# Kernel optimization log

Hardware: AMD Instinct MI355X
Metric: run time of the kernel (lower is better)

## Reference

```python
import jax, jax.numpy as jnp
import numpy as np

B, H, W, R, C = 4, 64, 64, 64, 32  # batch, height, width, in-channels r, conv out-channels


def setup_inputs() -> dict:
    key = jax.random.key(0)
    kx, kf, kg = jax.random.split(key, 3)
    x = jax.random.normal(kx, (B, H, W, R), dtype=jnp.float32)
    # 1x1 conv with in_channels=1: kernel is effectively a length-C vector
    w_f = jax.random.normal(kf, (C,), dtype=jnp.float32) * 0.1
    w_g = jax.random.normal(kg, (C,), dtype=jnp.float32) * 0.1
    gamma = jnp.ones((), dtype=jnp.float32)
    return {"x": x, "w_f": w_f, "w_g": w_g, "gamma": gamma}


def reference(x, w_f, w_g, gamma):
    b, h, w, r = x.shape
    hw = h * w
    xs = x.reshape(b, hw, r)                      # [B, HW, R]
    # conv_f / conv_g: each scalar of xs times weight vector -> [B, HW, R*C]
    x_f = (xs[..., None] * w_f).reshape(b, hw, -1)
    x_g = (xs[..., None] * w_g).reshape(b, hw, -1)
    attn = jnp.einsum('bik,bjk->bij', x_f, x_g)   # [B, HW, HW]
    attn = jax.nn.softmax(attn, axis=-1) * gamma
    # out[b,j,r] = sum_i attn[b,j,i] * xs[b,i,r]
    out = jnp.einsum('bji,bir->bjr', attn, xs)
    return out.reshape(b, h, w, r)
```

## Files before the change

### kernel.cpp

```cpp
#include <hip/hip_runtime.h>


#define N_SEQ 4096
#define KS    8
#define LOG2E 1.4426950408889634f

typedef __attribute__((ext_vector_type(8))) short short8;
typedef __attribute__((ext_vector_type(4))) short short4v;
typedef __attribute__((ext_vector_type(4))) float f4;
typedef __attribute__((ext_vector_type(16))) float f32x16;
typedef _Float16 half8  __attribute__((ext_vector_type(8)));
typedef _Float16 half2t __attribute__((ext_vector_type(2)));
typedef __fp16   fp16x2 __attribute__((ext_vector_type(2)));

union U8  { short8 v8; short4v v4[2]; unsigned short u[8]; };
union PKU { fp16x2 f; half2t h; unsigned int u; };
union US  { short8 s; half8 h; };
union W4U { unsigned int u[4]; half8 h; };

#define MFMA16(a,b,c)  __builtin_amdgcn_mfma_f32_16x16x32_bf16(a,b,c,0,0,0)
#define MFMA32F(a,b,c) __builtin_amdgcn_mfma_f32_32x32x16_f16(a,b,c,0,0,0)

static __device__ __forceinline__ unsigned short f2bf(float f){
  unsigned int u = __float_as_uint(f);
  u += 0x7fffu + ((u>>16)&1u);
  return (unsigned short)(u>>16);
}
static __device__ __forceinline__ float bf2f(unsigned short b){
  return __uint_as_float(((unsigned int)b)<<16);
}
static __device__ __forceinline__ unsigned int pk_u32(float a, float b){
#if __has_builtin(__builtin_amdgcn_cvt_pkrtz)
  PKU u; u.f = __builtin_amdgcn_cvt_pkrtz(a, b); return u.u;
#else
  PKU u; u.h.x = (_Float16)a; u.h.y = (_Float16)b; return u.u;
#endif
}
static __device__ __forceinline__ float fexp2(float x){
#if __has_builtin(__builtin_amdgcn_exp2f)
  return __builtin_amdgcn_exp2f(x);
#else
  return exp2f(x);
#endif
}
static __device__ __forceinline__ f4 splat4(float v){ f4 r; r.x=v; r.y=v; r.z=v; r.w=v; return r; }
static __device__ __forceinline__ f4 exp2v(f4 v){
  f4 r; r.x=fexp2(v.x); r.y=fexp2(v.y); r.z=fexp2(v.z); r.w=fexp2(v.w); return r;
}
static __device__ __forceinline__ f4 max4(f4 a, f4 b){
  f4 r; r.x=fmaxf(a.x,b.x); r.y=fmaxf(a.y,b.y); r.z=fmaxf(a.z,b.z); r.w=fmaxf(a.w,b.w); return r;
}
static __device__ __forceinline__ f4 shx4(f4 v, int m){
  f4 r; r.x=__shfl_xor(v.x,m,64); r.y=__shfl_xor(v.y,m,64);
        r.z=__shfl_xor(v.z,m,64); r.w=__shfl_xor(v.w,m,64); return r;
}
static __device__ __forceinline__ f32x16 zero16(){
  f32x16 z;
  #pragma unroll
  for (int i = 0; i < 16; ++i) z[i] = 0.f;
  return z;
}
static __device__ __forceinline__ void gload16(const unsigned short* g, unsigned short* l){
  __builtin_amdgcn_global_load_lds((const __attribute__((address_space(1))) void*)g,
                                   (__attribute__((address_space(3))) void*)l, 16, 0, 0);
}
static __device__ __forceinline__ half8 mkfrag(unsigned int Da0, unsigned int Da1,
                                               unsigned int Db0, unsigned int Db1, bool hib){
  const unsigned int e0 = __shfl_xor(hib ? Da0 : Db0, 32, 64);
  const unsigned int e1 = __shfl_xor(hib ? Da1 : Db1, 32, 64);
  W4U w;
  w.u[0] = hib ? e0  : Da0;
  w.u[1] = hib ? e1  : Da1;
  w.u[2] = hib ? Db0 : e0;
  w.u[3] = hib ? Db1 : e1;
  return w.h;
}

__global__ __launch_bounds__(256) void prep6_kernel(
    const float* __restrict__ x,
    unsigned short* __restrict__ XF, unsigned short* __restrict__ VF)
{
  __shared__ __align__(16) unsigned short T [64][82];
  __shared__ __align__(16) unsigned short TT[64][82];
  const int tid  = threadIdx.x;
  const int bb   = blockIdx.x >> 6;
  const int tile = blockIdx.x & 63;
  {
    const int r  = tid >> 2;
    const int c4 = tid & 3;
    const float* src = x + ((size_t)(bb*N_SEQ + tile*64 + r))*64 + c4*16;
    unsigned short h[16];
    #pragma unroll
    for (int i = 0; i < 4; ++i) {
      const float4 f = *(const float4*)(src + i*4);
      const unsigned int u0 = pk_u32(f.x, f.y);
      const unsigned int u1 = pk_u32(f.z, f.w);
      h[i*4+0] = (unsigned short)(u0 & 0xffffu);
      h[i*4+1] = (unsigned short)(u0 >> 16);
      h[i*4+2] = (unsigned short)(u1 & 0xffffu);
      h[i*4+3] = (unsigned short)(u1 >> 16);
    }
    #pragma unroll
    for (int j = 0; j < 16; ++j) T[r][c4*16+j] = h[j];
    #pragma unroll
    for (int j = 0; j < 16; ++j) TT[c4*16+j][r] = h[j];
  }
  __syncthreads();
  const size_t ob = ((size_t)(bb*64 + tile)) * 4096;
  #pragma unroll
  for (int s0 = 0; s0 < 2; ++s0) {
    const int s  = s0*256 + tid;
    const int fb = s >> 6;
    const int l  = s & 63;
    const int rr = (fb >> 2)*32 + (l & 31);
    const int cc = (fb & 3)*16 + (l >> 5)*8;
    U8 a, b;
    #pragma unroll
    for (int j = 0; j < 8; ++j) { a.u[j] = T[rr][cc+j]; b.u[j] = TT[rr][cc+j]; }
    *(short8*)(XF + ob + (size_t)s*8) = a.v8;
    *(short8*)(VF + ob + (size_t)s*8) = b.v8;
  }
}

__global__ __launch_bounds__(256, 2) void fattn8_kernel(
    const float* __restrict__ wf, const float* __restrict__ wg,
    const unsigned short* __restrict__ XF, const unsigned short* __restrict__ VF,
    float* __restrict__ OP, float* __restrict__ LP)
{
  __shared__ __align__(16) unsigned short KL[2][4096];
  __shared__ __align__(16) unsigned short VL[2][4096];

  const int tid  = threadIdx.x;
  const int lane = tid & 63;
  const int wv   = tid >> 6;
  const int l31  = lane & 31;
  const int hi   = lane >> 5;
  const bool hib = hi != 0;
  const int ks   = blockIdx.x >> 6;
  const int rem  = blockIdx.x & 63;
  const int bb   = rem >> 4;
  const int qP   = rem & 15;

  float s = 0.f;
  #pragma unroll
  for (int i = 0; i < 32; ++i) s += wf[i]*wg[i];
  const float s2 = s * LOG2E;
  const _Float16 s2h = (_Float16)s2;

  half8 qf[2][4];
  {
    const unsigned short* xq = XF + ((size_t)(bb*64 + qP*4 + wv))*4096 + lane*8;
    half8 sv;
    #pragma unroll
    for (int j = 0; j < 8; ++j) sv[j] = s2h;
    #pragma unroll
    for (int qg = 0; qg < 2; ++qg)
      #pragma unroll
      for (int kst = 0; kst < 4; ++kst) {
        US u; u.s = *(const short8*)(xq + (qg*4+kst)*512);
        qf[qg][kst] = u.h * sv;
      }
  }

  f32x16 Oc[2][2];
  #pragma unroll
  for (int qg = 0; qg < 2; ++qg)
    #pragma unroll
    for (int dg = 0; dg < 2; ++dg) Oc[qg][dg] = zero16();
  float lacc[2] = {0.f, 0.f};

  const unsigned short* gK = XF + ((size_t)(bb*64 + ks*8))*4096;
  const unsigned short* gV = VF + ((size_t)(bb*64 + ks*8))*4096;

  #pragma unroll
  for (int c = 0; c < 2; ++c) {
    gload16(gK + (c*256+tid)*8, &KL[0][(c*256+tid)*8]);
    gload16(gV + (c*256+tid)*8, &VL[0][(c*256+tid)*8]);
  }
  __syncthreads();

  #pragma unroll 1
  for (int it = 0; it < 8; ++it) {
    const int cur = it & 1;
    if (it + 1 < 8) {
      #pragma unroll
      for (int c = 0; c < 2; ++c) {
        gload16(gK + (it+1)*4096 + (c*256+tid)*8, &KL[cur^1][(c*256+tid)*8]);
        gload16(gV + (it+1)*4096 + (c*256+tid)*8, &VL[cur^1][(c*256+tid)*8]);
      }
    }
    const unsigned short* KB = &KL[cur][0];
    const unsigned short* VB = &VL[cur][0];

    #pragma unroll
    for (int kg = 0; kg < 2; ++kg) {
      half8 kf[4];
      #pragma unroll
      for (int kst = 0; kst < 4; ++kst) {
        US u; u.s = *(const short8*)(KB + ((kg*4+kst)*64 + lane)*8);
        kf[kst] = u.h;
      }
      f32x16 St[2];
      St[0] = zero16(); St[1] = zero16();
      __builtin_amdgcn_s_setprio(1);
      #pragma unroll
      for (int kst = 0; kst < 4; ++kst) {
        St[0] = MFMA32F(kf[kst], qf[0][kst], St[0]);
        St[1] = MFMA32F(kf[kst], qf[1][kst], St[1]);
      }
      __builtin_amdgcn_s_setprio(0);

      half8 pa[2][2];
      #pragma unroll
      for (int qg = 0; qg < 2; ++qg) {
        float p[16];
        float sm = 0.f;
        #pragma unroll
        for (int r = 0; r < 16; ++r) { p[r] = fexp2(St[qg][r]); sm += p[r]; }
        lacc[qg] += sm;
        const unsigned int D0 = pk_u32(p[0],  p[1]);
        const unsigned int D1 = pk_u32(p[2],  p[3]);
        const unsigned int D2 = pk_u32(p[4],  p[5]);
        const unsigned int D3 = pk_u32(p[6],  p[7]);
        const unsigned int D4 = pk_u32(p[8],  p[9]);
        const unsigned int D5 = pk_u32(p[10], p[11]);
        const unsigned int D6 = pk_u32(p[12], p[13]);
        const unsigned int D7 = pk_u32(p[14], p[15]);
        pa[qg][0] = mkfrag(D0, D1, D2, D3, hib);
        pa[qg][1] = mkfrag(D4, D5, D6, D7, hib);
      }

      __builtin_amdgcn_s_setprio(1);
      #pragma unroll
      for (int dg = 0; dg < 2; ++dg) {
        US v0, v1;
        v0.s = *(const short8*)(VB + ((dg*4 + kg*2 + 0)*64 + lane)*8);
        v1.s = *(const short8*)(VB + ((dg*4 + kg*2 + 1)*64 + lane)*8);
        #pragma unroll
        for (int qg = 0; qg < 2; ++qg) {
          Oc[qg][dg] = MFMA32F(pa[qg][0], v0.h, Oc[qg][dg]);
          Oc[qg][dg] = MFMA32F(pa[qg][1], v1.h, Oc[qg][dg]);
        }
      }
      __builtin_amdgcn_s_setprio(0);
    }
    __syncthreads();
  }

  lacc[0] += __shfl_xor(lacc[0], 32, 64);
  lacc[1] += __shfl_xor(lacc[1], 32, 64);

  float* op = OP + (size_t)blockIdx.x * (256*64);
  #pragma unroll
  for (int qg = 0; qg < 2; ++qg) {
    #pragma unroll
    for (int dg = 0; dg < 2; ++dg) {
      #pragma unroll
      for (int r = 0; r < 16; ++r) {
        const int row = wv*64 + qg*32 + (r & 3) + 8*(r >> 2) + 4*hi;
        op[row*64 + dg*32 + l31] = Oc[qg][dg][r];
      }
    }
    if (hi == 0)
      LP[(size_t)blockIdx.x*256 + wv*64 + qg*32 + l31] = lacc[qg];
  }
}

__global__ __launch_bounds__(256) void merge8_kernel(
    const float* __restrict__ OP, const float* __restrict__ LP,
    const float* __restrict__ gm, float* __restrict__ out)
{
  const int idx = blockIdx.x*256 + threadIdx.x;
  const int e0  = idx*4;
  const int d0  = e0 & 63;
  const int q   = e0 >> 6;
  const int bb  = q >> 12;
  const int qq  = q & 4095;
  const int qP  = qq >> 8;
  const int row = qq & 255;
  float4 acc = make_float4(0.f,0.f,0.f,0.f);
  float l = 0.f;
  #pragma unroll
  for (int sct = 0; sct < KS; ++sct) {
    const int blk = sct*64 + bb*16 + qP;
    const float4 o = *(const float4*)(OP + (size_t)blk*16384 + row*64 + d0);
    acc.x += o.x; acc.y += o.y; acc.z += o.z; acc.w += o.w;
    l += LP[(size_t)blk*256 + row];
  }
  const float w = gm[0] / l;
  float4 r; r.x = acc.x*w; r.y = acc.y*w; r.z = acc.z*w; r.w = acc.w*w;
  *(float4*)(out + e0) = r;
}

#define LDKF 72
#define TILEF (64*LDKF)
#define LDP 36

__global__ __launch_bounds__(256) void fattn_fallback(
    const float* __restrict__ x, const float* __restrict__ wf,
    const float* __restrict__ wg, const float* __restrict__ gm,
    float* __restrict__ out)
{
  __shared__ __align__(16) unsigned short KHI[2*TILEF];
  __shared__ __align__(16) unsigned short KLO[2*TILEF];
  __shared__ __align__(16) unsigned short VT [2*TILEF];
  __shared__ __align__(16) unsigned short PB [4*32*LDP];

  const int tid  = threadIdx.x;
  const int lane = tid & 63;
  const int wv   = tid >> 6;
  const int mg   = wv & 1;
  const int hh   = wv >> 1;
  const int quad = lane >> 4;
  const int l15  = lane & 15;
  const int bb   = blockIdx.x >> 6;
  const int qb   = (blockIdx.x & 63) << 6;

  float s = 0.f;
  #pragma unroll
  for (int i = 0; i < 32; ++i) s += wf[i]*wg[i];
  const float s2 = s * LOG2E;
  const float gamma = gm[0];

  const float* xb = x + ((size_t)bb * N_SEQ) * 64;

  short8 qhf[2][2], qlf[2][2];
  #pragma unroll
  for (int mt = 0; mt < 2; ++mt) {
    const int row = qb + mg*32 + mt*16 + l15;
    #pragma unroll
    for (int c = 0; c < 2; ++c) {
      const float* src = xb + row*64 + c*32 + quad*8;
      const float4 a0 = *(const float4*)src;
      const float4 a1 = *(const float4*)(src+4);
      float qv[8] = {a0.x,a0.y,a0.z,a0.w,a1.x,a1.y,a1.z,a1.w};
      U8 vh, vl;
      #pragma unroll
      for (int j = 0; j < 8; ++j) {
        float q = qv[j]*s2;
        unsigned short hb = f2bf(q);
        vh.u[j] = (short)hb;
        vl.u[j] = (short)f2bf(q - bf2f(hb));
      }
      qhf[mt][c] = vh.v8; qlf[mt][c] = vl.v8;
    }
  }

  f4 Oc[2][4], mo[2], ls[2];
  #pragma unroll
  for (int mt = 0; mt < 2; ++mt) {
    mo[mt] = splat4(-1e30f);
    ls[mt] = splat4(0.f);
    #pragma unroll
    for (int nt = 0; nt < 4; ++nt) Oc[mt][nt] = splat4(0.f);
  }

  const int sh   = tid >> 7;
  const int srow = (tid & 127) >> 1;
  const int sch  = tid & 1;

  float4 sr[8];
  {
    const float* sp = xb + (sh*2048 + srow)*64 + sch*32;
    #pragma unroll
    for (int i = 0; i < 8; ++i) sr[i] = *(const float4*)(sp + i*4);
    unsigned short hb[32], lb[32];
    #pragma unroll
    for (int i = 0; i < 8; ++i) {
      float vv[4] = {sr[i].x, sr[i].y, sr[i].z, sr[i].w};
      #pragma unroll
      for (int j = 0; j < 4; ++j) {
        unsigned short h = f2bf(vv[j]);
        hb[i*4+j] = h;
        lb[i*4+j] = f2bf(vv[j] - bf2f(h));
      }
    }
    const int kbase = sh*TILEF + srow*LDKF + sch*32;
    #pragma unroll
    for (int g = 0; g < 4; ++g) {
      U8 wh, wl;
      #pragma unroll
      for (int j = 0; j < 8; ++j) { wh.u[j]=(short)hb[g*8+j]; wl.u[j]=(short)lb[g*8+j]; }
      *(short8*)&KHI[kbase+g*8] = wh.v8;
      *(short8*)&KLO[kbase+g*8] = wl.v8;
    }
    #pragma unroll
    for (int j = 0; j < 32; ++j) VT[sh*TILEF + (sch*32+j)*LDKF + srow] = hb[j];
  }
  __syncthreads();

  #pragma unroll 1
  for (int t = 0; t < 32; ++t) {
    if (t+1 < 32) {
      const float* sp = xb + (sh*2048 + (t+1)*64 + srow)*64 + sch*32;
      #pragma unroll
      for (int i = 0; i < 8; ++i) sr[i] = *(const float4*)(sp + i*4);
    }

    f4 Sa[2][4];
    #pragma unroll
    for (int mt = 0; mt < 2; ++mt)
      #pragma unroll
      for (int n = 0; n < 4; ++n) Sa[mt][n] = splat4(0.f);

    const int kldsb = hh*TILEF;
    #pragma unroll
    for (int n = 0; n < 4; ++n) {
      #pragma unroll
      for (int c = 0; c < 2; ++c) {
        const int off = kldsb + (n*16 + l15)*LDKF + c*32 + quad*8;
        const short8 bh = *(const short8*)&KHI[off];
        const short8 bl = *(const short8*)&KLO[off];
        #pragma unroll
        for (int mt = 0; mt < 2; ++mt) {
          Sa[mt][n] = MFMA16(qhf[mt][c], bh, Sa[mt][n]);
          Sa[mt][n] = MFMA16(qlf[mt][c], bh, Sa[mt][n]);
          Sa[mt][n] = MFMA16(qhf[mt][c], bl, Sa[mt][n]);
        }
      }
    }

    f4 p[2][4];
    #pragma unroll
    for (int mt = 0; mt < 2; ++mt) {
      f4 rm = max4(max4(Sa[mt][0],Sa[mt][1]), max4(Sa[mt][2],Sa[mt][3]));
      rm = max4(rm, shx4(rm,1));
      rm = max4(rm, shx4(rm,2));
      rm = max4(rm, shx4(rm,4));
      rm = max4(rm, shx4(rm,8));
      f4 mn = max4(mo[mt], rm);
      f4 al = exp2v(mo[mt] - mn);
      mo[mt] = mn;
      f4 rs = splat4(0.f);
      #pragma unroll
      for (int n = 0; n < 4; ++n) { p[mt][n] = exp2v(Sa[mt][n] - mn); rs += p[mt][n]; }
      rs += shx4(rs,1); rs += shx4(rs,2); rs += shx4(rs,4); rs += shx4(rs,8);
      ls[mt] = ls[mt]*al + rs;
      #pragma unroll
      for (int nt = 0; nt < 4; ++nt) Oc[mt][nt] *= al;
    }

    const int pw = wv * (32*LDP);
    #pragma unroll
    for (int kc = 0; kc < 2; ++kc) {
      #pragma unroll
      for (int mt = 0; mt < 2; ++mt) {
        #pragma unroll
        for (int n2 = 0; n2 < 2; ++n2) {
          const f4 pv = p[mt][kc*2+n2];
          const int base = pw + (mt*16 + quad*4)*LDP + n2*16 + l15;
          ((unsigned short*)PB)[base        ] = f2bf(pv.x);
          ((unsigned short*)PB)[base +   LDP] = f2bf(pv.y);
          ((unsigned short*)PB)[base + 2*LDP] = f2bf(pv.z);
          ((unsigned short*)PB)[base + 3*LDP] = f2bf(pv.w);
        }
      }
      short8 pa[2];
      #pragma unroll
      for (int mt = 0; mt < 2; ++mt) {
        U8 u;
        const int rb = pw + (mt*16 + l15)*LDP + quad*8;
        u.v4[0] = *(const short4v*)&((unsigned short*)PB)[rb];
        u.v4[1] = *(const short4v*)&((unsigned short*)PB)[rb+4];
        pa[mt] = u.v8;
      }
      #pragma unroll
      for (int nt = 0; nt < 4; ++nt) {
        const short8 vb = *(const short8*)&VT[kldsb + (nt*16 + l15)*LDKF + kc*32 + quad*8];
        #pragma unroll
        for (int mt = 0; mt < 2; ++mt) Oc[mt][nt] = MFMA16(pa[mt], vb, Oc[mt][nt]);
      }
    }

    __syncthreads();

    if (t+1 < 32) {
      unsigned short hb[32], lb[32];
      #pragma unroll
      for (int i = 0; i < 8; ++i) {
        float vv[4] = {sr[i].x, sr[i].y, sr[i].z, sr[i].w};
        #pragma unroll
        for (int j = 0; j < 4; ++j) {
          unsigned short h = f2bf(vv[j]);
          hb[i*4+j] = h;
          lb[i*4+j] = f2bf(vv[j] - bf2f(h));
        }
      }
      const int kbase = sh*TILEF + srow*LDKF + sch*32;
      #pragma unroll
      for (int g = 0; g < 4; ++g) {
        U8 wh, wl;
        #pragma unroll
        for (int j = 0; j < 8; ++j) { wh.u[j]=(short)hb[g*8+j]; wl.u[j]=(short)lb[g*8+j]; }
        *(short8*)&KHI[kbase+g*8] = wh.v8;
        *(short8*)&KLO[kbase+g*8] = wl.v8;
      }
      #pragma unroll
      for (int j = 0; j < 32; ++j) VT[sh*TILEF + (sch*32+j)*LDKF + srow] = hb[j];
      __syncthreads();
    }
  }

  float* MO  = (float*)KHI;
  float* MML = (float*)KLO;
  if (hh == 1) {
    #pragma unroll
    for (int mt = 0; mt < 2; ++mt) {
      const int rbase = mg*32 + mt*16 + quad*4;
      #pragma unroll
      for (int nt = 0; nt < 4; ++nt) {
        MO[(rbase+0)*64 + nt*16 + l15] = Oc[mt][nt].x;
        MO[(rbase+1)*64 + nt*16 + l15] = Oc[mt][nt].y;
        MO[(rbase+2)*64 + nt*16 + l15] = Oc[mt][nt].z;
        MO[(rbase+3)*64 + nt*16 + l15] = Oc[mt][nt].w;
      }
      if (l15 == 0) {
        MML[rbase+0] = mo[mt].x; MML[rbase+1] = mo[mt].y;
        MML[rbase+2] = mo[mt].z; MML[rbase+3] = mo[mt].w;
        MML[64+rbase+0] = ls[mt].x; MML[64+rbase+1] = ls[mt].y;
        MML[64+rbase+2] = ls[mt].z; MML[64+rbase+3] = ls[mt].w;
      }
    }
  }
  __syncthreads();
  if (hh == 0) {
    #pragma unroll
    for (int mt = 0; mt < 2; ++mt) {
      const int rbase = mg*32 + mt*16 + quad*4;
      f4 m1, l1;
      m1.x = MML[rbase+0]; m1.y = MML[rbase+1]; m1.z = MML[rbase+2]; m1.w = MML[rbase+3];
      l1.x = MML[64+rbase+0]; l1.y = MML[64+rbase+1]; l1.z = MML[64+rbase+2]; l1.w = MML[64+rbase+3];
      const f4 mn = max4(mo[mt], m1);
      const f4 a0 = exp2v(mo[mt] - mn);
      const f4 a1 = exp2v(m1 - mn);
      f4 lt = ls[mt]*a0 + l1*a1;
      f4 w; w.x = gamma/lt.x; w.y = gamma/lt.y; w.z = gamma/lt.z; w.w = gamma/lt.w;
      #pragma unroll
      for (int nt = 0; nt < 4; ++nt) {
        #pragma unroll
        for (int rg = 0; rg < 4; ++rg) {
          const int rr = rbase + rg;
          const float o1 = MO[rr*64 + nt*16 + l15];
          const float val = (Oc[mt][nt][rg]*a0[rg] + o1*a1[rg]) * w[rg];
          out[((size_t)bb*N_SEQ + qb + rr)*64 + nt*16 + l15] = val;
        }
      }
    }
  }
}

extern "C" void kernel_launch(void* const* d_in, const int* in_sizes, int n_in,
                              void* d_out, int out_size, void* d_ws, size_t ws_size,
                              hipStream_t stream) {
  const float* x  = (const float*)d_in[0];
  const float* wf = (const float*)d_in[1];
  const float* wg = (const float*)d_in[2];
  const float* gm = (const float*)d_in[3];
  float* out = (float*)d_out;

  const size_t XF_OFF = 0;
  const size_t VF_OFF = 2097152;
  const size_t OP_OFF = 4194304;
  const size_t LP_OFF = OP_OFF + (size_t)512*256*64*4;
  const size_t NEED   = LP_OFF + (size_t)512*256*4;

  if (ws_size >= NEED) {
    unsigned short* XFp = (unsigned short*)((char*)d_ws + XF_OFF);
    unsigned short* VFp = (unsigned short*)((char*)d_ws + VF_OFF);
    float* OP = (float*)((char*)d_ws + OP_OFF);
    float* LP = (float*)((char*)d_ws + LP_OFF);
    prep6_kernel<<<dim3(256), dim3(256), 0, stream>>>(x, XFp, VFp);
    fattn8_kernel<<<dim3(512), dim3(256), 0, stream>>>(wf, wg, XFp, VFp, OP, LP);
    merge8_kernel<<<dim3(1024), dim3(256), 0, stream>>>(OP, LP, gm, out);
  } else {
    fattn_fallback<<<dim3(256), dim3(256), 0, stream>>>(x, wf, wg, gm, out);
  }
}
```

Before: 93.75 us.

## Replace global split-K with intra-block wave split and fused merge

The attention kernel no longer splits the key sequence across 8 blocks that write partial outputs and row sums to global memory for a separate merge kernel. Instead, 256 blocks of 512 threads each own 64 queries and sweep all keys. Waves are split by key parity, key group and query group, and their partial results are reduced through shared memory before the kernel writes normalized output directly. This removes the merge launch and the global round-trip of partials, in exchange for fewer, larger blocks, a 65 KB shared buffer, and longer serial loops per block.

```diff
diff --git a/kernel.cpp b/kernel.cpp
--- a/kernel.cpp
+++ b/kernel.cpp
@@ -2,7 +2,6 @@
 
 
 #define N_SEQ 4096
-#define KS    8
 #define LOG2E 1.4426950408889634f
 
 typedef __attribute__((ext_vector_type(8))) short short8;
@@ -122,13 +121,16 @@
   }
 }
 
-__global__ __launch_bounds__(256, 2) void fattn8_kernel(
+__global__ __launch_bounds__(512, 2) void fattn9_kernel(
     const float* __restrict__ wf, const float* __restrict__ wg,
+    const float* __restrict__ gm,
     const unsigned short* __restrict__ XF, const unsigned short* __restrict__ VF,
-    float* __restrict__ OP, float* __restrict__ LP)
+    float* __restrict__ out)
 {
-  __shared__ __align__(16) unsigned short KL[2][4096];
-  __shared__ __align__(16) unsigned short VL[2][4096];
+  __shared__ __align__(16) unsigned char SMEM[66560];
+  unsigned short* TLE  = (unsigned short*)SMEM;
+  float*          LO   = (float*)SMEM;
+  float*          LSUM = (float*)(SMEM + 65536);
 
   const int tid  = threadIdx.x;
   const int lane = tid & 63;
@@ -136,10 +138,11 @@
   const int l31  = lane & 31;
   const int hi   = lane >> 5;
   const bool hib = hi != 0;
-  const int ks   = blockIdx.x >> 6;
-  const int rem  = blockIdx.x & 63;
-  const int bb   = rem >> 4;
-  const int qP   = rem & 15;
+  const int par  = wv >> 2;
+  const int kg   = (wv >> 1) & 1;
+  const int qg   = wv & 1;
+  const int bb   = blockIdx.x >> 6;
+  const int qt   = blockIdx.x & 63;
 
   float s = 0.f;
   #pragma unroll
@@ -147,149 +150,125 @@
   const float s2 = s * LOG2E;
   const _Float16 s2h = (_Float16)s2;
 
-  half8 qf[2][4];
+  half8 qf[4];
   {
-    const unsigned short* xq = XF + ((size_t)(bb*64 + qP*4 + wv))*4096 + lane*8;
+    const unsigned short* xq = XF + ((size_t)(bb*64 + qt))*4096 + lane*8;
     half8 sv;
     #pragma unroll
     for (int j = 0; j < 8; ++j) sv[j] = s2h;
     #pragma unroll
-    for (int qg = 0; qg < 2; ++qg)
-      #pragma unroll
-      for (int kst = 0; kst < 4; ++kst) {
-        US u; u.s = *(const short8*)(xq + (qg*4+kst)*512);
-        qf[qg][kst] = u.h * sv;
-      }
-  }
-
-  f32x16 Oc[2][2];
-  #pragma unroll
-  for (int qg = 0; qg < 2; ++qg)
-    #pragma unroll
-    for (int dg = 0; dg < 2; ++dg) Oc[qg][dg] = zero16();
-  float lacc[2] = {0.f, 0.f};
-
-  const unsigned short* gK = XF + ((size_t)(bb*64 + ks*8))*4096;
-  const unsigned short* gV = VF + ((size_t)(bb*64 + ks*8))*4096;
-
-  #pragma unroll
-  for (int c = 0; c < 2; ++c) {
-    gload16(gK + (c*256+tid)*8, &KL[0][(c*256+tid)*8]);
-    gload16(gV + (c*256+tid)*8, &VL[0][(c*256+tid)*8]);
-  }
+    for (int kst = 0; kst < 4; ++kst) {
+      US u; u.s = *(const short8*)(xq + (qg*4+kst)*512);
+      qf[kst] = u.h * sv;
+    }
+  }
+
+  f32x16 Oc[2];
+  Oc[0] = zero16(); Oc[1] = zero16();
+  float lacc = 0.f;
+
+  const unsigned short* gK = XF + (size_t)bb*64*4096;
+  const unsigned short* gV = VF + (size_t)bb*64*4096;
+
+  #define STAGE(p, b)                                                            \
+    _Pragma("unroll")                                                            \
+    for (int c = 0; c < 4; ++c) {                                                \
+      const unsigned short* src =                                                \
+        ((c >> 1) ? gV : gK) + ((size_t)((p)*2 + (c & 1)))*4096 + tid*8;         \
+      unsigned short* dst = TLE + ((((b)*2 + (c & 1))*2 + (c >> 1))*4096) + tid*8;\
+      gload16(src, dst);                                                         \
+    }
+
+  STAGE(0, 0);
   __syncthreads();
 
   #pragma unroll 1
-  for (int it = 0; it < 8; ++it) {
+  for (int it = 0; it < 32; ++it) {
     const int cur = it & 1;
-    if (it + 1 < 8) {
-      #pragma unroll
-      for (int c = 0; c < 2; ++c) {
-        gload16(gK + (it+1)*4096 + (c*256+tid)*8, &KL[cur^1][(c*256+tid)*8]);
-        gload16(gV + (it+1)*4096 + (c*256+tid)*8, &VL[cur^1][(c*256+tid)*8]);
-      }
-    }
-    const unsigned short* KB = &KL[cur][0];
-    const unsigned short* VB = &VL[cur][0];
-
-    #pragma unroll
-    for (int kg = 0; kg < 2; ++kg) {
-      half8 kf[4];
-      #pragma unroll
-      for (int kst = 0; kst < 4; ++kst) {
-        US u; u.s = *(const short8*)(KB + ((kg*4+kst)*64 + lane)*8);
-        kf[kst] = u.h;
-      }
-      f32x16 St[2];
-      St[0] = zero16(); St[1] = zero16();
-      __builtin_amdgcn_s_setprio(1);
-      #pragma unroll
-      for (int kst = 0; kst < 4; ++kst) {
-        St[0] = MFMA32F(kf[kst], qf[0][kst], St[0]);
-        St[1] = MFMA32F(kf[kst], qf[1][kst], St[1]);
-      }
-      __builtin_amdgcn_s_setprio(0);
-
-      half8 pa[2][2];
-      #pragma unroll
-      for (int qg = 0; qg < 2; ++qg) {
-        float p[16];
-        float sm = 0.f;
-        #pragma unroll
-        for (int r = 0; r < 16; ++r) { p[r] = fexp2(St[qg][r]); sm += p[r]; }
-        lacc[qg] += sm;
-        const unsigned int D0 = pk_u32(p[0],  p[1]);
-        const unsigned int D1 = pk_u32(p[2],  p[3]);
-        const unsigned int D2 = pk_u32(p[4],  p[5]);
-        const unsigned int D3 = pk_u32(p[6],  p[7]);
-        const unsigned int D4 = pk_u32(p[8],  p[9]);
-        const unsigned int D5 = pk_u32(p[10], p[11]);
-        const unsigned int D6 = pk_u32(p[12], p[13]);
-        const unsigned int D7 = pk_u32(p[14], p[15]);
-        pa[qg][0] = mkfrag(D0, D1, D2, D3, hib);
-        pa[qg][1] = mkfrag(D4, D5, D6, D7, hib);
-      }
-
-      __builtin_amdgcn_s_setprio(1);
-      #pragma unroll
-      for (int dg = 0; dg < 2; ++dg) {
-        US v0, v1;
-        v0.s = *(const short8*)(VB + ((dg*4 + kg*2 + 0)*64 + lane)*8);
-        v1.s = *(const short8*)(VB + ((dg*4 + kg*2 + 1)*64 + lane)*8);
-        #pragma unroll
-        for (int qg = 0; qg < 2; ++qg) {
-          Oc[qg][dg] = MFMA32F(pa[qg][0], v0.h, Oc[qg][dg]);
-          Oc[qg][dg] = MFMA32F(pa[qg][1], v1.h, Oc[qg][dg]);
-        }
-      }
-      __builtin_amdgcn_s_setprio(0);
-    }
+    if (it + 1 < 32) { STAGE(it + 1, cur ^ 1); }
+
+    const unsigned short* KB = TLE + ((cur*2 + par)*2 + 0)*4096;
+    const unsigned short* VB = KB + 4096;
+
+    half8 kf[4];
+    #pragma unroll
+    for (int kst = 0; kst < 4; ++kst) {
+      US u; u.s = *(const short8*)(KB + ((kg*4+kst)*64 + lane)*8);
+      kf[kst] = u.h;
+    }
+    f32x16 St = zero16();
+    __builtin_amdgcn_s_setprio(1);
+    #pragma unroll
+    for (int kst = 0; kst < 4; ++kst) St = MFMA32F(kf[kst], qf[kst], St);
+    __builtin_amdgcn_s_setprio(0);
+
+    float p[16];
+    float sm = 0.f;
+    #pragma unroll
+    for (int r = 0; r < 16; ++r) { p[r] = fexp2(St[r]); sm += p[r]; }
+    lacc += sm;
+    const unsigned int D0 = pk_u32(p[0],  p[1]);
+    const unsigned int D1 = pk_u32(p[2],  p[3]);
+    const unsigned int D2 = pk_u32(p[4],  p[5]);
+    const unsigned int D3 = pk_u32(p[6],  p[7]);
+    const unsigned int D4 = pk_u32(p[8],  p[9]);
+    const unsigned int D5 = pk_u32(p[10], p[11]);
+    const unsigned int D6 = pk_u32(p[12], p[13]);
+    const unsigned int D7 = pk_u32(p[14], p[15]);
+    half8 pa0 = mkfrag(D0, D1, D2, D3, hib);
+    half8 pa1 = mkfrag(D4, D5, D6, D7, hib);
+
+    __builtin_amdgcn_s_setprio(1);
+    #pragma unroll
+    for (int dg = 0; dg < 2; ++dg) {
+      US v0, v1;
+      v0.s = *(const short8*)(VB + ((dg*4 + kg*2 + 0)*64 + lane)*8);
+      v1.s = *(const short8*)(VB + ((dg*4 + kg*2 + 1)*64 + lane)*8);
+      Oc[dg] = MFMA32F(pa0, v0.h, Oc[dg]);
+      Oc[dg] = MFMA32F(pa1, v1.h, Oc[dg]);
+    }
+    __builtin_amdgcn_s_setprio(0);
+
     __syncthreads();
   }
 
-  lacc[0] += __shfl_xor(lacc[0], 32, 64);
-  lacc[1] += __shfl_xor(lacc[1], 32, 64);
-
-  float* op = OP + (size_t)blockIdx.x * (256*64);
-  #pragma unroll
-  for (int qg = 0; qg < 2; ++qg) {
-    #pragma unroll
-    for (int dg = 0; dg < 2; ++dg) {
-      #pragma unroll
-      for (int r = 0; r < 16; ++r) {
-        const int row = wv*64 + qg*32 + (r & 3) + 8*(r >> 2) + 4*hi;
-        op[row*64 + dg*32 + l31] = Oc[qg][dg][r];
-      }
-    }
-    if (hi == 0)
-      LP[(size_t)blockIdx.x*256 + wv*64 + qg*32 + l31] = lacc[qg];
-  }
-}
-
-__global__ __launch_bounds__(256) void merge8_kernel(
-    const float* __restrict__ OP, const float* __restrict__ LP,
-    const float* __restrict__ gm, float* __restrict__ out)
-{
-  const int idx = blockIdx.x*256 + threadIdx.x;
-  const int e0  = idx*4;
-  const int d0  = e0 & 63;
-  const int q   = e0 >> 6;
-  const int bb  = q >> 12;
-  const int qq  = q & 4095;
-  const int qP  = qq >> 8;
-  const int row = qq & 255;
-  float4 acc = make_float4(0.f,0.f,0.f,0.f);
-  float l = 0.f;
-  #pragma unroll
-  for (int sct = 0; sct < KS; ++sct) {
-    const int blk = sct*64 + bb*16 + qP;
-    const float4 o = *(const float4*)(OP + (size_t)blk*16384 + row*64 + d0);
-    acc.x += o.x; acc.y += o.y; acc.z += o.z; acc.w += o.w;
-    l += LP[(size_t)blk*256 + row];
-  }
-  const float w = gm[0] / l;
-  float4 r; r.x = acc.x*w; r.y = acc.y*w; r.z = acc.z*w; r.w = acc.w*w;
-  *(float4*)(out + e0) = r;
+  lacc += __shfl_xor(lacc, 32, 64);
+
+  #pragma unroll
+  for (int dg = 0; dg < 2; ++dg)
+    #pragma unroll
+    for (int r = 0; r < 16; ++r) {
+      const int ql = (r & 3) + 8*(r >> 2) + 4*hi;
+      LO[wv*2048 + ql*64 + dg*32 + l31] = Oc[dg][r];
+    }
+  if (hi == 0) LSUM[wv*32 + l31] = lacc;
+  __syncthreads();
+
+  {
+    const float gamma = gm[0];
+    const int r  = tid >> 3;
+    const int d0 = (tid & 7)*8;
+    const int q  = r & 31;
+    const int qr = r >> 5;
+    const float l = LSUM[(qr+0)*32 + q] + LSUM[(qr+2)*32 + q]
+                  + LSUM[(qr+4)*32 + q] + LSUM[(qr+6)*32 + q];
+    const float w = gamma / l;
+    float acc[8];
+    #pragma unroll
+    for (int j = 0; j < 8; ++j) acc[j] = 0.f;
+    #pragma unroll
+    for (int j = 0; j < 4; ++j) {
+      const float* src = LO + (qr + j*2)*2048 + q*64 + d0;
+      #pragma unroll
+      for (int e = 0; e < 8; ++e) acc[e] += src[e];
+    }
+    float4 r0, r1;
+    r0.x = acc[0]*w; r0.y = acc[1]*w; r0.z = acc[2]*w; r0.w = acc[3]*w;
+    r1.x = acc[4]*w; r1.y = acc[5]*w; r1.z = acc[6]*w; r1.w = acc[7]*w;
+    float* dst = out + ((size_t)(bb*N_SEQ + qt*64 + r))*64 + d0;
+    *(float4*)dst = r0;
+    *(float4*)(dst + 4) = r1;
+  }
 }
 
 #define LDKF 72
@@ -560,18 +539,13 @@
 
   const size_t XF_OFF = 0;
   const size_t VF_OFF = 2097152;
-  const size_t OP_OFF = 4194304;
-  const size_t LP_OFF = OP_OFF + (size_t)512*256*64*4;
-  const size_t NEED   = LP_OFF + (size_t)512*256*4;
+  const size_t NEED   = 4194304;
 
   if (ws_size >= NEED) {
     unsigned short* XFp = (unsigned short*)((char*)d_ws + XF_OFF);
     unsigned short* VFp = (unsigned short*)((char*)d_ws + VF_OFF);
-    float* OP = (float*)((char*)d_ws + OP_OFF);
-    float* LP = (float*)((char*)d_ws + LP_OFF);
     prep6_kernel<<<dim3(256), dim3(256), 0, stream>>>(x, XFp, VFp);
-    fattn8_kernel<<<dim3(512), dim3(256), 0, stream>>>(wf, wg, XFp, VFp, OP, LP);
-    merge8_kernel<<<dim3(1024), dim3(256), 0, stream>>>(OP, LP, gm, out);
+    fattn9_kernel<<<dim3(256), dim3(512), 0, stream>>>(wf, wg, gm, XFp, VFp, out);
   } else {
     fattn_fallback<<<dim3(256), dim3(256), 0, stream>>>(x, wf, wg, gm, out);
   }
```

After: 97.51 us. 1.04x slower.
